# Kernel optimization log

Hardware: AMD Instinct MI355X
Metric: run time of the kernel (lower is better)

## Reference

```python
import jax, jax.numpy as jnp
import numpy as np

D = 128

def setup_inputs() -> dict:
    key = jax.random.key(0)
    k1, k2, k3, k4, k5, k6, k7 = jax.random.split(key, 7)
    B, L = 2048, 200
    target = jax.random.normal(k1, (B, D), dtype=jnp.float32)
    item_seq = jax.random.normal(k2, (B, L, D), dtype=jnp.float32)
    seq_len = jax.random.randint(k3, (B,), 0, 200, dtype=jnp.int64 if jax.config.jax_enable_x64 else jnp.int32)
    # MLP params: Linear(4D -> 2D), Linear(2D -> 1), PyTorch-style init scale
    s1 = 1.0 / np.sqrt(4 * D)
    s2 = 1.0 / np.sqrt(2 * D)
    W1 = jax.random.uniform(k4, (4 * D, 2 * D), minval=-s1, maxval=s1, dtype=jnp.float32)
    b1 = jax.random.uniform(k5, (2 * D,), minval=-s1, maxval=s1, dtype=jnp.float32)
    W2 = jax.random.uniform(k6, (2 * D, 1), minval=-s2, maxval=s2, dtype=jnp.float32)
    b2 = jax.random.uniform(k7, (1,), minval=-s2, maxval=s2, dtype=jnp.float32)
    return {"target": target, "item_seq": item_seq, "seq_len": seq_len,
            "W1": W1, "b1": b1, "W2": W2, "b2": b2}

def reference(target, item_seq, seq_len, W1, b1, W2, b2):
    B, L, Dd = item_seq.shape
    t = target[:, None, :]                              # B 1 D (broadcast over L)
    tgt = jnp.broadcast_to(t, (B, L, Dd))
    sub = item_seq - tgt
    dot = item_seq * tgt
    mlp_in = jnp.concatenate([tgt, item_seq, sub, dot], axis=-1)   # B L 4D
    h = jax.nn.relu(jnp.einsum('blf,fh->blh', mlp_in, W1) + b1)    # B L 2D
    score = jnp.einsum('blh,ho->blo', h, W2) + b2                  # B L 1
    mask = (jnp.arange(L)[None, :] < seq_len[:, None]).astype(item_seq.dtype)  # B L
    weighted = score * item_seq * mask[:, :, None]                 # B L D
    return jnp.sum(weighted, axis=1)                               # B D
```

## Files before the change

kernel.cpp:

```cpp
#include <hip/hip_runtime.h>
#include <hip/hip_bf16.h>

typedef short short8 __attribute__((ext_vector_type(8)));
typedef float f32x4 __attribute__((ext_vector_type(4)));

#define XS 136

static __device__ inline short f2bf(float f) {
    unsigned u = __float_as_uint(f);
    unsigned r = (u + 0x7fffu + ((u >> 16) & 1u)) >> 16;
    return (short)r;
}
static __device__ inline float bf2f(short s) {
    return __uint_as_float(((unsigned)(unsigned short)s) << 16);
}
static __device__ inline unsigned cvtpk(float lo, float hi) {
    unsigned r;
    asm("v_cvt_pk_bf16_f32 %0, %1, %2" : "=v"(r) : "v"(lo), "v"(hi));
    return r;
}

__global__ void precompute(const float* __restrict__ W1, const float* __restrict__ b1,
                           const float* __restrict__ target, short* __restrict__ Wbc,
                           short* __restrict__ Wd, float* __restrict__ U) {
    __shared__ float tl[1024];
    const int tid = threadIdx.x;
    if (blockIdx.x >= 256) {
        int idx = (blockIdx.x - 256) * 256 + tid;
        int half = idx >> 15;
        int i = idx & 32767;
        int j = i & 7;
        int l = (i >> 3) & 63;
        int s = (i >> 9) & 3;
        int t = i >> 11;
        int k = s * 32 + ((l >> 4) << 3) + j;
        int n = t * 16 + (l & 15);
        if (half == 0) Wbc[i] = f2bf(W1[(128 + k) * 256 + n] + W1[(256 + k) * 256 + n]);
        else           Wd[i]  = f2bf(W1[(384 + k) * 256 + n]);
        return;
    }
    const int b8 = blockIdx.x;
#pragma unroll
    for (int k = 0; k < 4; k++) tl[k * 256 + tid] = target[b8 * 1024 + k * 256 + tid];
    __syncthreads();
    float acc[8] = {0.f, 0.f, 0.f, 0.f, 0.f, 0.f, 0.f, 0.f};
#pragma unroll 8
    for (int d = 0; d < 128; ++d) {
        float wud = W1[d * 256 + tid] - W1[(256 + d) * 256 + tid];
#pragma unroll
        for (int r = 0; r < 8; r++) acc[r] += tl[r * 128 + d] * wud;
    }
    float bj = b1[tid];
#pragma unroll
    for (int r = 0; r < 8; r++) U[(b8 * 8 + r) * 256 + tid] = acc[r] + bj;
}

__launch_bounds__(256, 2)
__global__ void din_main(const float* __restrict__ target, const float* __restrict__ item_seq,
                         const int* __restrict__ seq_len, const float* __restrict__ W2,
                         const float* __restrict__ b2p, const short* __restrict__ Wbc,
                         const short* __restrict__ Wd, const float* __restrict__ U,
                         float* __restrict__ out) {
    const int b = blockIdx.x;
    const int tid = threadIdx.x;
    const int lane = tid & 63;
    const int w = tid >> 6;
    const int col = lane & 15;
    const int q = lane >> 4;

    const int slen = seq_len[b];
    const int nt = (slen + 15) >> 4;

    __shared__ __attribute__((aligned(16))) short Xl[4][16 * XS];
    __shared__ __attribute__((aligned(16))) float tsh[128];
    __shared__ float u_s[256];
    __shared__ float w2_s[256];
    __shared__ __attribute__((aligned(16))) float scoreP[2][16][4];
    __shared__ float out_s[128];

    const int r = tid >> 4;
    const int c = (tid & 15) << 3;

    float4 v0, v1;
    {
        const float4* src = (const float4*)(item_seq + (((size_t)b * 200 + r) * 128 + c));
        v0 = src[0]; v1 = src[1];
    }

    if (tid < 128) tsh[tid] = target[b * 128 + tid];
    u_s[tid] = U[b * 256 + tid];
    w2_s[tid] = W2[tid];
    const float b2 = b2p[0];
    __syncthreads();

    short8 bfrag[4][4];
#pragma unroll
    for (int s = 0; s < 4; s++) {
        const float4* tp = (const float4*)(tsh + s * 32 + q * 8);
        float4 ta = tp[0], tb = tp[1];
        float tk[8] = {ta.x, ta.y, ta.z, ta.w, tb.x, tb.y, tb.z, tb.w};
#pragma unroll
        for (int i = 0; i < 4; i++) {
            size_t off = ((size_t)((w * 4 + i) * 4 + s) * 64 + lane) * 8;
            short8 bc = *(const short8*)(Wbc + off);
            short8 dd = *(const short8*)(Wd + off);
            float f0 = fmaf(tk[0], bf2f(dd[0]), bf2f(bc[0]));
            float f1 = fmaf(tk[1], bf2f(dd[1]), bf2f(bc[1]));
            float f2 = fmaf(tk[2], bf2f(dd[2]), bf2f(bc[2]));
            float f3 = fmaf(tk[3], bf2f(dd[3]), bf2f(bc[3]));
            float f4 = fmaf(tk[4], bf2f(dd[4]), bf2f(bc[4]));
            float f5 = fmaf(tk[5], bf2f(dd[5]), bf2f(bc[5]));
            float f6 = fmaf(tk[6], bf2f(dd[6]), bf2f(bc[6]));
            float f7 = fmaf(tk[7], bf2f(dd[7]), bf2f(bc[7]));
            uint4 pe;
            pe.x = cvtpk(f0, f1);
            pe.y = cvtpk(f2, f3);
            pe.z = cvtpk(f4, f5);
            pe.w = cvtpk(f6, f7);
            bfrag[i][s] = *(short8*)&pe;
        }
    }

    float u_c[4], w2c[4];
#pragma unroll
    for (int i = 0; i < 4; i++) {
        int j = (w * 4 + i) * 16 + col;
        u_c[i] = u_s[j];
        w2c[i] = w2_s[j];
    }

    const int d = tid & 127;
    const int g = tid >> 7;
    float out_val = 0.f;

    auto accum_tile = [&](int pt) {
        const short* xp = Xl[pt & 3];
        const int l0p = pt * 16;
        const float4* spb = (const float4*)scoreP[pt & 1];
#pragma unroll
        for (int mm = 0; mm < 8; mm++) {
            int m = g * 8 + mm;
            int l = l0p + m;
            float4 sp = spb[m];
            float s = (sp.x + sp.y) + (sp.z + sp.w) + b2;
            s = (l < slen) ? s : 0.f;
            out_val = fmaf(s, bf2f(xp[m * XS + d]), out_val);
        }
    };

    for (int mt = 0; mt < nt; ++mt) {
        short* xb = Xl[mt & 3];

        {
            uint4 pk;
            pk.x = cvtpk(v0.x, v0.y);
            pk.y = cvtpk(v0.z, v0.w);
            pk.z = cvtpk(v1.x, v1.y);
            pk.w = cvtpk(v1.z, v1.w);
            *(uint4*)(xb + r * XS + c) = pk;
        }
        __syncthreads();

        if (mt + 1 < nt) {
            int lr = (mt + 1) * 16 + r;
            if (lr > 199) lr = 199;
            const float4* src = (const float4*)(item_seq + (((size_t)b * 200 + lr) * 128 + c));
            v0 = src[0]; v1 = src[1];
        }

        f32x4 acc[4];
#pragma unroll
        for (int i = 0; i < 4; i++) acc[i] = (f32x4){u_c[i], u_c[i], u_c[i], u_c[i]};
        const short* arow = xb + col * XS + q * 8;
#pragma unroll
        for (int s = 0; s < 4; s++) {
            short8 af = *(const short8*)(arow + s * 32);
#pragma unroll
            for (int i = 0; i < 4; i++)
                acc[i] = __builtin_amdgcn_mfma_f32_16x16x32_bf16(af, bfrag[i][s], acc[i], 0, 0, 0);
        }

        float sv[4];
#pragma unroll
        for (int rg = 0; rg < 4; rg++) {
            float s0 = 0.f;
#pragma unroll
            for (int i = 0; i < 4; i++) {
                float h = acc[i][rg];
                h = h > 0.f ? h : 0.f;
                s0 = fmaf(h, w2c[i], s0);
            }
            sv[rg] = s0;
        }
#pragma unroll
        for (int off = 1; off < 16; off <<= 1) {
#pragma unroll
            for (int rg = 0; rg < 4; rg++) sv[rg] += __shfl_xor(sv[rg], off, 64);
        }
        if (col == 0) {
#pragma unroll
            for (int rg = 0; rg < 4; rg++) scoreP[mt & 1][q * 4 + rg][w] = sv[rg];
        }

        if (mt > 0) accum_tile(mt - 1);
    }

    if (nt > 0) {
        __syncthreads();
        accum_tile(nt - 1);
    }

    __syncthreads();
    if (g == 1) out_s[d] = out_val;
    __syncthreads();
    if (g == 0) out[b * 128 + d] = out_val + out_s[d];
}

extern "C" void kernel_launch(void* const* d_in, const int* in_sizes, int n_in,
                              void* d_out, int out_size, void* d_ws, size_t ws_size,
                              hipStream_t stream) {
    const float* target   = (const float*)d_in[0];
    const float* item_seq = (const float*)d_in[1];
    const int*   seq_len  = (const int*)d_in[2];
    const float* W1       = (const float*)d_in[3];
    const float* b1       = (const float*)d_in[4];
    const float* W2       = (const float*)d_in[5];
    const float* b2       = (const float*)d_in[6];
    float* out = (float*)d_out;

    char* ws = (char*)d_ws;
    short* Wbc = (short*)ws;
    short* Wd  = (short*)(ws + 65536);
    float* U   = (float*)(ws + 131072);

    precompute<<<512, 256, 0, stream>>>(W1, b1, target, Wbc, Wd, U);
    din_main<<<2048, 256, 0, stream>>>(target, item_seq, seq_len, W2, b2, Wbc, Wd, U, out);
}
```

Measured before the change: 300.9 us.

## Early-exit empty sequences, load params directly, vectorize weighted-sum accumulation

Blocks with zero sequence length now write zeros and return immediately, so they skip the weight-fragment setup. Target, U and W2 are read straight from global memory into registers, which removes the shared-memory staging and one barrier. The per-tile weighted sum now has each thread handle four contiguous D columns over two rows, using 8-byte LDS loads. The eight partial sums are reduced through a larger shared buffer at the end, which adds a bit of LDS traffic.

```diff
diff --git a/kernel.cpp b/kernel.cpp
--- a/kernel.cpp
+++ b/kernel.cpp
@@ -71,32 +71,41 @@
     const int slen = seq_len[b];
     const int nt = (slen + 15) >> 4;
 
+    if (nt == 0) {
+        if (tid < 128) out[b * 128 + tid] = 0.f;
+        return;
+    }
+
     __shared__ __attribute__((aligned(16))) short Xl[4][16 * XS];
-    __shared__ __attribute__((aligned(16))) float tsh[128];
-    __shared__ float u_s[256];
-    __shared__ float w2_s[256];
     __shared__ __attribute__((aligned(16))) float scoreP[2][16][4];
-    __shared__ float out_s[128];
+    __shared__ __attribute__((aligned(16))) float outr[8][128];
 
     const int r = tid >> 4;
     const int c = (tid & 15) << 3;
 
+    const float* item_b = item_seq + ((size_t)b * 200 + r) * 128 + c;
+
     float4 v0, v1;
     {
-        const float4* src = (const float4*)(item_seq + (((size_t)b * 200 + r) * 128 + c));
+        const float4* src = (const float4*)item_b;
         v0 = src[0]; v1 = src[1];
     }
 
-    if (tid < 128) tsh[tid] = target[b * 128 + tid];
-    u_s[tid] = U[b * 256 + tid];
-    w2_s[tid] = W2[tid];
     const float b2 = b2p[0];
-    __syncthreads();
+
+    float u_c[4], w2c[4];
+#pragma unroll
+    for (int i = 0; i < 4; i++) {
+        int j = (w * 4 + i) * 16 + col;
+        u_c[i] = U[b * 256 + j];
+        w2c[i] = W2[j];
+    }
 
     short8 bfrag[4][4];
+    const float* tgt = target + b * 128;
 #pragma unroll
     for (int s = 0; s < 4; s++) {
-        const float4* tp = (const float4*)(tsh + s * 32 + q * 8);
+        const float4* tp = (const float4*)(tgt + s * 32 + q * 8);
         float4 ta = tp[0], tb = tp[1];
         float tk[8] = {ta.x, ta.y, ta.z, ta.w, tb.x, tb.y, tb.z, tb.w};
 #pragma unroll
@@ -121,30 +130,28 @@
         }
     }
 
-    float u_c[4], w2c[4];
-#pragma unroll
-    for (int i = 0; i < 4; i++) {
-        int j = (w * 4 + i) * 16 + col;
-        u_c[i] = u_s[j];
-        w2c[i] = w2_s[j];
-    }
-
-    const int d = tid & 127;
-    const int g = tid >> 7;
-    float out_val = 0.f;
+    const int qd = tid & 31;
+    const int gg = tid >> 5;
+    f32x4 ov = (f32x4){0.f, 0.f, 0.f, 0.f};
 
     auto accum_tile = [&](int pt) {
         const short* xp = Xl[pt & 3];
         const int l0p = pt * 16;
-        const float4* spb = (const float4*)scoreP[pt & 1];
-#pragma unroll
-        for (int mm = 0; mm < 8; mm++) {
-            int m = g * 8 + mm;
-            int l = l0p + m;
-            float4 sp = spb[m];
+#pragma unroll
+        for (int rr = 0; rr < 2; rr++) {
+            int m = gg * 2 + rr;
+            float4 sp = *(const float4*)&scoreP[pt & 1][m][0];
             float s = (sp.x + sp.y) + (sp.z + sp.w) + b2;
-            s = (l < slen) ? s : 0.f;
-            out_val = fmaf(s, bf2f(xp[m * XS + d]), out_val);
+            s = (l0p + m < slen) ? s : 0.f;
+            uint2 xv = *(const uint2*)(xp + m * XS + 4 * qd);
+            float x0 = __uint_as_float(xv.x << 16);
+            float x1 = __uint_as_float(xv.x & 0xffff0000u);
+            float x2 = __uint_as_float(xv.y << 16);
+            float x3 = __uint_as_float(xv.y & 0xffff0000u);
+            ov[0] = fmaf(s, x0, ov[0]);
+            ov[1] = fmaf(s, x1, ov[1]);
+            ov[2] = fmaf(s, x2, ov[2]);
+            ov[3] = fmaf(s, x3, ov[3]);
         }
     };
 
@@ -164,7 +171,7 @@
         if (mt + 1 < nt) {
             int lr = (mt + 1) * 16 + r;
             if (lr > 199) lr = 199;
-            const float4* src = (const float4*)(item_seq + (((size_t)b * 200 + lr) * 128 + c));
+            const float4* src = (const float4*)(item_b + ((size_t)(lr - r)) * 128);
             v0 = src[0]; v1 = src[1];
         }
 
@@ -205,15 +212,17 @@
         if (mt > 0) accum_tile(mt - 1);
     }
 
-    if (nt > 0) {
-        __syncthreads();
-        accum_tile(nt - 1);
-    }
-
     __syncthreads();
-    if (g == 1) out_s[d] = out_val;
+    accum_tile(nt - 1);
+
+    *(float4*)&outr[gg][4 * qd] = *(float4*)&ov;
     __syncthreads();
-    if (g == 0) out[b * 128 + d] = out_val + out_s[d];
+    if (tid < 128) {
+        float s = 0.f;
+#pragma unroll
+        for (int k = 0; k < 8; k++) s += outr[k][tid];
+        out[b * 128 + tid] = s;
+    }
 }
 
 extern "C" void kernel_launch(void* const* d_in, const int* in_sizes, int n_in,
```

Result: no change. 298.2 us (median of 2 runs) (-0.9%).
